# Optimization experiments

Measured on AMD Instinct MI355X. Metric: run time of the kernel, lower is better.

The kernel has to match this reference:

```python
import jax, jax.numpy as jnp
import numpy as np

S, L, T, E, H = 512, 5, 20, 768, 64


def setup_inputs() -> dict:
    key = jax.random.key(0)
    ks = jax.random.split(key, 32)

    def p(k, shape, scale=0.05):
        return jax.random.normal(k, shape, dtype=jnp.float32) * scale

    return {
        "text_input": jax.random.normal(ks[0], (S, L, T, E), dtype=jnp.float32),
        "time_inputs": jax.random.uniform(ks[1], (S, L, T), dtype=jnp.float32),
        # TimeLSTM per-stock params (gate order f, i, o, c_tmp)
        "Wall": p(ks[2], (S, H, 4 * H)), "bWall": p(ks[3], (S, 4 * H)),
        "Uall": p(ks[4], (S, E, 4 * H)), "bUall": p(ks[5], (S, 4 * H)),
        "Wd": p(ks[6], (S, H, H)), "bWd": p(ks[7], (S, H)),
        # shared text/day Attention per stock
        "W1": p(ks[8], (S, H, H)), "b1": p(ks[9], (S, H)),
        "W2": p(ks[10], (S, H, H)), "b2": p(ks[11], (S, H)),
        "V": p(ks[12], (S, H, 1)), "bV": p(ks[13], (S, 1)),
        # day nn.LSTM per stock (gate order i, f, g, o)
        "Wih": p(ks[14], (S, H, 4 * H)), "Whh": p(ks[15], (S, H, 4 * H)),
        "bih": p(ks[16], (S, 4 * H)), "bhh": p(ks[17], (S, 4 * H)),
        # shared output head
        "lin_w": p(ks[18], (H, 1)), "lin_b": p(ks[19], (1,)),
        "no_stocks": S,
    }


def _forward(text_input, time_inputs, Wall, bWall, Uall, bUall, Wd, bWd,
             W1, b1, W2, b2, V, bV, Wih, Whh, bih, bhh, lin_w, lin_b, no_stocks):
    def per_stock(x, ts, Wall, bWall, Uall, bUall, Wd, bWd,
                  W1, b1, W2, b2, V, bV, Wih, Whh, bih, bhh):
        # x: [L, T, E], ts: [L, T] -- lookback days are an inner batch for the TimeLSTM
        u = jnp.einsum('lte,eg->ltg', x, Uall) + bUall  # [L, T, 4H]

        def step(carry, inp):
            h, c = carry                 # [L, H]
            u_t, ts_t = inp              # [L, 4H], [L]
            c_s1 = jnp.tanh(c @ Wd + bWd)
            c_adj = (c - c_s1) + c_s1 * ts_t[:, None]
            gates = h @ Wall + bWall + u_t
            f, i, o, c_tmp = jnp.split(gates, 4, axis=1)
            f = jax.nn.sigmoid(f)
            i = jax.nn.sigmoid(i)
            o = jax.nn.sigmoid(o)
            c_tmp = jax.nn.sigmoid(c_tmp)  # sigmoid (not tanh), faithful to source
            c_new = f * c_adj + i * c_tmp
            h_new = o * jnp.tanh(c_new)
            return (h_new, c_new), o     # module collects the o gate as 'outputs'

        init = (jnp.zeros((L, H), x.dtype), jnp.zeros((L, H), x.dtype))
        (h_fin, _), o_seq = jax.lax.scan(step, init, (u.transpose(1, 0, 2), ts.T))
        full = o_seq.transpose(1, 0, 2)  # [L, T, H]

        # text attention: score = V(tanh(W1(last) + W2(full))), softmax over T
        score = jnp.tanh((h_fin @ W1 + b1)[:, None, :] + full @ W2 + b2) @ V + bV  # [L, T, 1]
        aw = jax.nn.softmax(score, axis=1)
        text_vec = jnp.sum(aw * full, axis=1)  # [L, H]

        # day nn.LSTM: input (1, L, H) seq-first => one cell step with batch=L, zero state
        h0 = jnp.zeros((L, H), x.dtype)
        g = text_vec @ Wih + bih + h0 @ Whh + bhh
        gi, gf, gg, go = jnp.split(g, 4, axis=1)
        c_d = jax.nn.sigmoid(gi) * jnp.tanh(gg)  # f * c0 = 0
        h_d = jax.nn.sigmoid(go) * jnp.tanh(c_d)  # [L, H]; output == h_n here

        # day attention reuses the SAME text_attention weights; full == last == h_d
        s2 = jnp.tanh(h_d @ W1 + b1 + h_d @ W2 + b2) @ V + bV  # [L, 1]
        aw2 = jax.nn.softmax(s2, axis=0)
        return jnp.sum(aw2 * h_d, axis=0)  # [H]

    ft_vec = jax.vmap(per_stock)(text_input, time_inputs, Wall, bWall, Uall, bUall,
                                 Wd, bWd, W1, b1, W2, b2, V, bV,
                                 Wih, Whh, bih, bhh)  # [S, H]
    return jax.nn.leaky_relu(ft_vec @ lin_w + lin_b, negative_slope=0.01)  # [S, 1]


def reference(text_input, time_inputs, Wall, bWall, Uall, bUall, Wd, bWd,
              W1, b1, W2, b2, V, bV, Wih, Whh, bih, bhh, lin_w, lin_b, no_stocks):
    return _forward(text_input, time_inputs, Wall, bWall, Uall, bUall, Wd, bWd,
                    W1, b1, W2, b2, V, bV, Wih, Whh, bih, bhh, lin_w, lin_b, no_stocks)
```

## Files before the change

kernel.cpp:

```cpp
#include <hip/hip_runtime.h>
#include <cstddef>

#define NS 512
#define NL 5
#define NT 20
#define NE 768
#define NH 64
#define NG 256

__device__ __forceinline__ float sigf(float x) { return 1.0f / (1.0f + expf(-x)); }
__device__ __forceinline__ float bcast(float v, int k) {
    return __int_as_float(__builtin_amdgcn_readlane(__float_as_int(v), k));
}

typedef __attribute__((ext_vector_type(8))) short short8v;
typedef __attribute__((ext_vector_type(4))) float f32x4;

__device__ __forceinline__ void split_bf16(float x, unsigned short& hi, unsigned short& lo) {
    unsigned int bx = __float_as_uint(x);
    unsigned int h = (bx + 0x8000u) >> 16;
    hi = (unsigned short)h;
    float r = x - __uint_as_float(h << 16);
    lo = (unsigned short)((__float_as_uint(r) + 0x8000u) >> 16);
}

__global__ __launch_bounds__(512, 2) void k_gemm_u(
    const float* __restrict__ x, const float* __restrict__ U,
    const float* __restrict__ bU, float* __restrict__ u)
{
    __shared__ unsigned short Af[8 * 2 * 64 * 8];
    __shared__ unsigned short Bf[16 * 2 * 64 * 8];
    const int s = blockIdx.x;
    const int tid = threadIdx.x;
    const int wave = tid >> 6, lane = tid & 63;
    const int wm = wave & 1, wn = wave >> 1;
    const float* xg = x + (size_t)s * (NL * NT * NE);
    const float* Ug = U + (size_t)s * (NE * NG);

    f32x4 acc[4][4] = {};

    const int arow = tid >> 2, ab = tid & 3;
    const unsigned int a_off0 = (((unsigned)(arow >> 4) * 2 + 0) * 64 + ((arow & 15) + 16 * ab)) * 8;
    const unsigned int a_off1 = a_off0 + 64 * 8;
    const int bcol = tid & 255, bq1 = tid >> 8;
    const unsigned int b_base = (unsigned)(bcol >> 4) * 2 * 64 * 8;
    const unsigned int b_off1h = b_base + ((bcol & 15) + 16 * bq1) * 8;
    const unsigned int b_off1l = b_off1h + 64 * 8;
    const unsigned int b_off2h = b_base + ((bcol & 15) + 16 * (bq1 + 2)) * 8;
    const unsigned int b_off2l = b_off2h + 64 * 8;

    float av[8], bv1[8], bv2[8];
    {
        const float* pa = xg + (size_t)arow * NE + ab * 8;
        if (arow < 100) {
            float4 q0 = *(const float4*)pa, q1 = *(const float4*)(pa + 4);
            av[0]=q0.x; av[1]=q0.y; av[2]=q0.z; av[3]=q0.w;
            av[4]=q1.x; av[5]=q1.y; av[6]=q1.z; av[7]=q1.w;
        } else {
            #pragma unroll
            for (int j = 0; j < 8; ++j) av[j] = 0.0f;
        }
        const float* pb = Ug + bcol;
        #pragma unroll
        for (int j = 0; j < 8; ++j) {
            bv1[j] = pb[(size_t)(8 * bq1 + j) * NG];
            bv2[j] = pb[(size_t)(8 * bq1 + 16 + j) * NG];
        }
    }

    for (int st = 0; st < 24; ++st) {
        {
            unsigned short h[8], l[8];
            #pragma unroll
            for (int j = 0; j < 8; ++j) split_bf16(av[j], h[j], l[j]);
            uint4 ph, pl;
            ph.x = h[0] | (h[1] << 16); ph.y = h[2] | (h[3] << 16);
            ph.z = h[4] | (h[5] << 16); ph.w = h[6] | (h[7] << 16);
            pl.x = l[0] | (l[1] << 16); pl.y = l[2] | (l[3] << 16);
            pl.z = l[4] | (l[5] << 16); pl.w = l[6] | (l[7] << 16);
            *(uint4*)&Af[a_off0] = ph;
            *(uint4*)&Af[a_off1] = pl;
            #pragma unroll
            for (int j = 0; j < 8; ++j) split_bf16(bv1[j], h[j], l[j]);
            ph.x = h[0] | (h[1] << 16); ph.y = h[2] | (h[3] << 16);
            ph.z = h[4] | (h[5] << 16); ph.w = h[6] | (h[7] << 16);
            pl.x = l[0] | (l[1] << 16); pl.y = l[2] | (l[3] << 16);
            pl.z = l[4] | (l[5] << 16); pl.w = l[6] | (l[7] << 16);
            *(uint4*)&Bf[b_off1h] = ph;
            *(uint4*)&Bf[b_off1l] = pl;
            #pragma unroll
            for (int j = 0; j < 8; ++j) split_bf16(bv2[j], h[j], l[j]);
            ph.x = h[0] | (h[1] << 16); ph.y = h[2] | (h[3] << 16);
            ph.z = h[4] | (h[5] << 16); ph.w = h[6] | (h[7] << 16);
            pl.x = l[0] | (l[1] << 16); pl.y = l[2] | (l[3] << 16);
            pl.z = l[4] | (l[5] << 16); pl.w = l[6] | (l[7] << 16);
            *(uint4*)&Bf[b_off2h] = ph;
            *(uint4*)&Bf[b_off2l] = pl;
        }
        __syncthreads();

        if (st + 1 < 24) {
            const int k0 = (st + 1) * 32;
            const float* pa = xg + (size_t)arow * NE + k0 + ab * 8;
            if (arow < 100) {
                float4 q0 = *(const float4*)pa, q1 = *(const float4*)(pa + 4);
                av[0]=q0.x; av[1]=q0.y; av[2]=q0.z; av[3]=q0.w;
                av[4]=q1.x; av[5]=q1.y; av[6]=q1.z; av[7]=q1.w;
            } else {
                #pragma unroll
                for (int j = 0; j < 8; ++j) av[j] = 0.0f;
            }
            const float* pb = Ug + (size_t)k0 * NG + bcol;
            #pragma unroll
            for (int j = 0; j < 8; ++j) {
                bv1[j] = pb[(size_t)(8 * bq1 + j) * NG];
                bv2[j] = pb[(size_t)(8 * bq1 + 16 + j) * NG];
            }
        }

        short8v ah[4], al[4];
        #pragma unroll
        for (int mi = 0; mi < 4; ++mi) {
            const unsigned int mt = wm * 4 + mi;
            ah[mi] = *(const short8v*)&Af[(mt * 2 + 0) * 512 + lane * 8];
            al[mi] = *(const short8v*)&Af[(mt * 2 + 1) * 512 + lane * 8];
        }
        #pragma unroll
        for (int ni = 0; ni < 4; ++ni) {
            const unsigned int nt = wn * 4 + ni;
            short8v bh = *(const short8v*)&Bf[(nt * 2 + 0) * 512 + lane * 8];
            short8v bl = *(const short8v*)&Bf[(nt * 2 + 1) * 512 + lane * 8];
            #pragma unroll
            for (int mi = 0; mi < 4; ++mi) {
                acc[mi][ni] = __builtin_amdgcn_mfma_f32_16x16x32_bf16(ah[mi], bh, acc[mi][ni], 0, 0, 0);
                acc[mi][ni] = __builtin_amdgcn_mfma_f32_16x16x32_bf16(ah[mi], bl, acc[mi][ni], 0, 0, 0);
                acc[mi][ni] = __builtin_amdgcn_mfma_f32_16x16x32_bf16(al[mi], bh, acc[mi][ni], 0, 0, 0);
            }
        }
        __syncthreads();
    }

    const int c_sub = 4 * (lane >> 4);
    #pragma unroll
    for (int ni = 0; ni < 4; ++ni) {
        const int gcol = wn * 64 + ni * 16 + (lane & 15);
        const float bb = bU[(size_t)s * NG + gcol];
        #pragma unroll
        for (int mi = 0; mi < 4; ++mi) {
            const int grow0 = wm * 64 + mi * 16 + c_sub;
            #pragma unroll
            for (int r = 0; r < 4; ++r) {
                const int grow = grow0 + r;
                if (grow < 100) {
                    const int ld = grow / 20, td = grow % 20;
                    u[(((size_t)s * NT + td) * NL + ld) * NG + gcol] = acc[mi][ni][r] + bb;
                }
            }
        }
    }
}

#define R_WD    0
#define R_GATES 4096
#define R_HS    5376
#define R_TS    5696
#define R_TOT   5796

__global__ __launch_bounds__(320, 4) void k_recur(
    float* __restrict__ u, const float* __restrict__ ti,
    const float* __restrict__ Wall, const float* __restrict__ bWall,
    const float* __restrict__ Wd, const float* __restrict__ bWd)
{
    __shared__ float sm[R_TOT];
    const int s = blockIdx.x;
    const int tid = threadIdx.x;
    const int lq = tid >> 6, hh = tid & 63;
    const int lane = hh;
    float* ug = u + (size_t)s * NT * NL * NG;

    for (int i = tid; i < 1024; i += 320)
        *(float4*)&sm[R_WD + i * 4] = *(const float4*)(Wd + (size_t)s * 4096 + i * 4);
    if (tid < NL * NT) sm[R_TS + tid] = ti[(size_t)s * NL * NT + tid];
    sm[R_HS + tid] = 0.0f;
    const float bwd_r = bWd[(size_t)s * NH + hh];
    float c_reg = 0.0f;
    float wall_r[NH];
    float bwall_r = 0.0f, uc[NL];
    if (tid < NG) {
        bwall_r = bWall[(size_t)s * NG + tid];
        const float* wp = Wall + (size_t)s * (NH * NG) + tid;
        #pragma unroll
        for (int k = 0; k < NH; ++k) wall_r[k] = wp[(size_t)k * NG];
        #pragma unroll
        for (int l = 0; l < NL; ++l) uc[l] = ug[(size_t)l * NG + tid];
    }
    __syncthreads();

    for (int t = 0; t < NT; ++t) {
        float un[NL];
        if (tid < NG) {
            if (t + 1 < NT) {
                #pragma unroll
                for (int l = 0; l < NL; ++l)
                    un[l] = ug[(size_t)((t + 1) * NL + l) * NG + tid];
            } else {
                #pragma unroll
                for (int l = 0; l < NL; ++l) un[l] = 0.0f;
            }
            float hreg[NL];
            #pragma unroll
            for (int l = 0; l < NL; ++l) hreg[l] = sm[R_HS + l * NH + lane];
            float gv[NL];
            #pragma unroll
            for (int l = 0; l < NL; ++l) gv[l] = bwall_r + uc[l];
            #pragma unroll
            for (int k = 0; k < NH; ++k) {
                float w = wall_r[k];
                #pragma unroll
                for (int l = 0; l < NL; ++l)
                    gv[l] += bcast(hreg[l], k) * w;
            }
            #pragma unroll
            for (int l = 0; l < NL; ++l)
                sm[R_GATES + l * NG + tid] = sigf(gv[l]);
        }
        float ssum = bwd_r;
        #pragma unroll
        for (int k = 0; k < NH; ++k)
            ssum += bcast(c_reg, k) * sm[R_WD + k * NH + hh];
        float cs1 = tanhf(ssum);
        float ca = c_reg - cs1 + cs1 * sm[R_TS + lq * NT + t];
        __syncthreads();
        {
            float f  = sm[R_GATES + lq * NG + hh];
            float ii = sm[R_GATES + lq * NG + 64 + hh];
            float oo = sm[R_GATES + lq * NG + 128 + hh];
            float ct = sm[R_GATES + lq * NG + 192 + hh];
            float cn = f * ca + ii * ct;
            c_reg = cn;
            sm[R_HS + tid] = oo * tanhf(cn);
            ug[(size_t)(t * NL + lq) * NG + hh] = oo;
        }
        __syncthreads();
        if (tid < NG) {
            #pragma unroll
            for (int l = 0; l < NL; ++l) uc[l] = un[l];
        }
    }
    ug[(size_t)(0 * NL + lq) * NG + 64 + hh] = sm[R_HS + tid];
}

#define P_W1    0
#define P_W2    4096
#define P_FULLO 8192
#define P_HS    14592
#define P_TQ    14912
#define P_CA    15232
#define P_SC    15552
#define P_B0    15652
#define P_B1    15716
#define P_BVV   15780
#define P_BV1   15844
#define P_TOT   15848

__global__ __launch_bounds__(320, 2) void k_post(
    const float* __restrict__ u,
    const float* __restrict__ W1, const float* __restrict__ b1,
    const float* __restrict__ W2, const float* __restrict__ b2,
    const float* __restrict__ V, const float* __restrict__ bV,
    const float* __restrict__ Wih, const float* __restrict__ bih,
    const float* __restrict__ bhh, const float* __restrict__ lin_w,
    const float* __restrict__ lin_b, float* __restrict__ out)
{
    __shared__ float sm[P_TOT];
    const int s = blockIdx.x;
    const int tid = threadIdx.x;
    const int lq = tid >> 6, hh = tid & 63;
    const int lane = hh;
    const float* ug = u + (size_t)s * NT * NL * NG;

    for (int i = tid; i < 1024; i += 320)
        *(float4*)&sm[P_W1 + i * 4] = *(const float4*)(W1 + (size_t)s * 4096 + i * 4);
    for (int i = tid; i < 1024; i += 320)
        *(float4*)&sm[P_W2 + i * 4] = *(const float4*)(W2 + (size_t)s * 4096 + i * 4);
    for (int i = tid; i < 1600; i += 320) {
        const int idx = i >> 4;
        const int l = idx / NT, t = idx % NT;
        const int k4 = (i & 15) * 4;
        *(float4*)&sm[P_FULLO + idx * NH + k4] =
            *(const float4*)(ug + (size_t)(t * NL + l) * NG + k4);
    }
    sm[P_HS + tid] = ug[(size_t)(0 * NL + lq) * NG + 64 + hh];
    if (tid < NH) {
        sm[P_B0 + tid]  = b1[(size_t)s * NH + tid];
        sm[P_B1 + tid]  = b2[(size_t)s * NH + tid];
        sm[P_BVV + tid] = V[(size_t)s * NH + tid];
    }
    if (tid == 0) sm[P_BV1] = bV[s];
    __syncthreads();

    {
        float qv = sm[P_B0 + hh];
        for (int k4 = 0; k4 < NH; k4 += 4) {
            float4 hv = *(const float4*)&sm[P_HS + lq * NH + k4];
            qv += hv.x * sm[P_W1 + (k4 + 0) * NH + hh]
                + hv.y * sm[P_W1 + (k4 + 1) * NH + hh]
                + hv.z * sm[P_W1 + (k4 + 2) * NH + hh]
                + hv.w * sm[P_W1 + (k4 + 3) * NH + hh];
        }
        sm[P_TQ + tid] = qv;
    }
    __syncthreads();

    for (int lt = lq; lt < NL * NT; lt += 5) {
        int l = lt / NT;
        float v = sm[P_TQ + l * NH + lane] + sm[P_B1 + lane];
        for (int k4 = 0; k4 < NH; k4 += 4) {
            float4 fv = *(const float4*)&sm[P_FULLO + lt * NH + k4];
            v += fv.x * sm[P_W2 + (k4 + 0) * NH + lane]
               + fv.y * sm[P_W2 + (k4 + 1) * NH + lane]
               + fv.z * sm[P_W2 + (k4 + 2) * NH + lane]
               + fv.w * sm[P_W2 + (k4 + 3) * NH + lane];
        }
        v = tanhf(v) * sm[P_BVV + lane];
        #pragma unroll
        for (int m = 32; m > 0; m >>= 1) v += __shfl_xor(v, m, 64);
        if (lane == 0) sm[P_SC + lt] = v + sm[P_BV1];
    }
    __syncthreads();

    if (tid < NL) {
        float mx = -1e30f;
        for (int t = 0; t < NT; ++t) mx = fmaxf(mx, sm[P_SC + tid * NT + t]);
        float sum = 0.0f;
        for (int t = 0; t < NT; ++t) {
            float e = expf(sm[P_SC + tid * NT + t] - mx);
            sm[P_SC + tid * NT + t] = e;
            sum += e;
        }
        float inv = 1.0f / sum;
        for (int t = 0; t < NT; ++t) sm[P_SC + tid * NT + t] *= inv;
    }
    __syncthreads();

    {
        float sv = 0.0f;
        #pragma unroll
        for (int t = 0; t < NT; ++t)
            sv += sm[P_SC + lq * NT + t] * sm[P_FULLO + (lq * NT + t) * NH + hh];
        sm[P_CA + tid] = sv;
    }
    __syncthreads();

    if (tid < NG) {
        float bsum = bih[(size_t)s * NG + tid] + bhh[(size_t)s * NG + tid];
        float d[NL];
        #pragma unroll
        for (int l = 0; l < NL; ++l) d[l] = bsum;
        for (int k = 0; k < NH; ++k) {
            float wk = Wih[((size_t)s * NH + k) * NG + tid];
            #pragma unroll
            for (int l = 0; l < NL; ++l)
                d[l] += sm[P_CA + l * NH + k] * wk;
        }
        #pragma unroll
        for (int l = 0; l < NL; ++l)
            sm[P_FULLO + l * NG + tid] = d[l];
    }
    __syncthreads();
    {
        float gi = sm[P_FULLO + lq * NG + hh];
        float gg = sm[P_FULLO + lq * NG + 128 + hh];
        float go = sm[P_FULLO + lq * NG + 192 + hh];
        float cd = sigf(gi) * tanhf(gg);
        sm[P_TQ + tid] = sigf(go) * tanhf(cd);
    }
    __syncthreads();

    {
        float v = sm[P_B0 + lane] + sm[P_B1 + lane];
        for (int k4 = 0; k4 < NH; k4 += 4) {
            float4 hv = *(const float4*)&sm[P_TQ + lq * NH + k4];
            v += hv.x * (sm[P_W1 + (k4 + 0) * NH + lane] + sm[P_W2 + (k4 + 0) * NH + lane])
               + hv.y * (sm[P_W1 + (k4 + 1) * NH + lane] + sm[P_W2 + (k4 + 1) * NH + lane])
               + hv.z * (sm[P_W1 + (k4 + 2) * NH + lane] + sm[P_W2 + (k4 + 2) * NH + lane])
               + hv.w * (sm[P_W1 + (k4 + 3) * NH + lane] + sm[P_W2 + (k4 + 3) * NH + lane]);
        }
        v = tanhf(v) * sm[P_BVV + lane];
        #pragma unroll
        for (int m = 32; m > 0; m >>= 1) v += __shfl_xor(v, m, 64);
        if (lane == 0) sm[P_SC + lq] = v + sm[P_BV1];
    }
    __syncthreads();
    if (tid == 0) {
        float mx = -1e30f;
        for (int l = 0; l < NL; ++l) mx = fmaxf(mx, sm[P_SC + l]);
        float sum = 0.0f;
        for (int l = 0; l < NL; ++l) {
            float e = expf(sm[P_SC + l] - mx);
            sm[P_SC + l] = e;
            sum += e;
        }
        float inv = 1.0f / sum;
        for (int l = 0; l < NL; ++l) sm[P_SC + l] *= inv;
    }
    __syncthreads();

    if (tid < NH) {
        float fv = 0.0f;
        #pragma unroll
        for (int l = 0; l < NL; ++l)
            fv += sm[P_SC + l] * sm[P_TQ + l * NH + tid];
        fv *= lin_w[tid];
        #pragma unroll
        for (int m = 32; m > 0; m >>= 1) fv += __shfl_xor(fv, m, 64);
        if (tid == 0) {
            float val = fv + lin_b[0];
            out[s] = val > 0.0f ? val : 0.01f * val;
        }
    }
}

extern "C" void kernel_launch(void* const* d_in, const int* in_sizes, int n_in,
                              void* d_out, int out_size, void* d_ws, size_t ws_size,
                              hipStream_t stream) {
    (void)in_sizes; (void)n_in; (void)out_size; (void)ws_size;
    const float* x     = (const float*)d_in[0];
    const float* ti    = (const float*)d_in[1];
    const float* Wall  = (const float*)d_in[2];
    const float* bWall = (const float*)d_in[3];
    const float* Uall  = (const float*)d_in[4];
    const float* bUall = (const float*)d_in[5];
    const float* Wd    = (const float*)d_in[6];
    const float* bWd   = (const float*)d_in[7];
    const float* W1    = (const float*)d_in[8];
    const float* b1    = (const float*)d_in[9];
    const float* W2    = (const float*)d_in[10];
    const float* b2    = (const float*)d_in[11];
    const float* V     = (const float*)d_in[12];
    const float* bV    = (const float*)d_in[13];
    const float* Wih   = (const float*)d_in[14];
    const float* bih   = (const float*)d_in[16];
    const float* bhh   = (const float*)d_in[17];
    const float* lin_w = (const float*)d_in[18];
    const float* lin_b = (const float*)d_in[19];
    float* out = (float*)d_out;
    float* u = (float*)d_ws;

    k_gemm_u<<<NS, 512, 0, stream>>>(x, Uall, bUall, u);
    k_recur<<<NS, 320, 0, stream>>>(u, ti, Wall, bWall, Wd, bWd);
    k_post<<<NS, 320, 0, stream>>>(u, W1, b1, W2, b2, V, bV,
                                   Wih, bih, bhh, lin_w, lin_b, out);
}
```

Measured before the change: 879.5 us.

## Split U-GEMM across two blocks, use fp16 split MFMA, LDS broadcasts in recurrence

The input-projection GEMM now runs two blocks per stock, each computing half of the 256 gate columns. This doubles the grid and raises launch_bounds occupancy to 4 blocks per CU. The hi/lo operand split moves from manual bf16 rounding to packed fp16 conversion (cvt_pkrtz) with fp16 MFMA, which cuts conversion ALU work and gives more mantissa bits, at some risk of fp16 range overflow. In the recurrence, readlane broadcasts of h and c are replaced by float4 LDS reads, with c kept in shared memory. This adds LDS traffic but removes the serial readlane chains.

New measurement: 873.1 us. Within noise of the previous version (-0.7%).

```diff
diff --git a/kernel.cpp b/kernel.cpp
--- a/kernel.cpp
+++ b/kernel.cpp
@@ -9,47 +9,54 @@
 #define NG 256
 
 __device__ __forceinline__ float sigf(float x) { return 1.0f / (1.0f + expf(-x)); }
-__device__ __forceinline__ float bcast(float v, int k) {
-    return __int_as_float(__builtin_amdgcn_readlane(__float_as_int(v), k));
-}
-
-typedef __attribute__((ext_vector_type(8))) short short8v;
+
+typedef __fp16 h16x2 __attribute__((ext_vector_type(2)));
+typedef _Float16 f16x8 __attribute__((ext_vector_type(8)));
 typedef __attribute__((ext_vector_type(4))) float f32x4;
 
-__device__ __forceinline__ void split_bf16(float x, unsigned short& hi, unsigned short& lo) {
-    unsigned int bx = __float_as_uint(x);
-    unsigned int h = (bx + 0x8000u) >> 16;
-    hi = (unsigned short)h;
-    float r = x - __uint_as_float(h << 16);
-    lo = (unsigned short)((__float_as_uint(r) + 0x8000u) >> 16);
-}
-
-__global__ __launch_bounds__(512, 2) void k_gemm_u(
+union PkU { h16x2 h; unsigned u; };
+
+__device__ __forceinline__ void split_pk(float a, float b, unsigned& hi, unsigned& lo) {
+    PkU H, L;
+    H.h = __builtin_amdgcn_cvt_pkrtz(a, b);
+    float ra = a - (float)H.h[0];
+    float rb = b - (float)H.h[1];
+    L.h = __builtin_amdgcn_cvt_pkrtz(ra, rb);
+    hi = H.u; lo = L.u;
+}
+
+__device__ __forceinline__ void stage8(const float v[8], unsigned short* base, unsigned off) {
+    uint4 ph, pl;
+    split_pk(v[0], v[1], ph.x, pl.x);
+    split_pk(v[2], v[3], ph.y, pl.y);
+    split_pk(v[4], v[5], ph.z, pl.z);
+    split_pk(v[6], v[7], ph.w, pl.w);
+    *(uint4*)&base[off]       = ph;
+    *(uint4*)&base[off + 512] = pl;
+}
+
+__global__ __launch_bounds__(512, 4) void k_gemm_u(
     const float* __restrict__ x, const float* __restrict__ U,
     const float* __restrict__ bU, float* __restrict__ u)
 {
-    __shared__ unsigned short Af[8 * 2 * 64 * 8];
-    __shared__ unsigned short Bf[16 * 2 * 64 * 8];
-    const int s = blockIdx.x;
+    __shared__ unsigned short Af[8 * 2 * 512];
+    __shared__ unsigned short Bf[8 * 2 * 512];
+    const int bid = blockIdx.x;
+    const int s = bid >> 1, half = bid & 1;
     const int tid = threadIdx.x;
     const int wave = tid >> 6, lane = tid & 63;
     const int wm = wave & 1, wn = wave >> 1;
     const float* xg = x + (size_t)s * (NL * NT * NE);
-    const float* Ug = U + (size_t)s * (NE * NG);
-
-    f32x4 acc[4][4] = {};
+    const float* Ug = U + (size_t)s * (NE * NG) + half * 128;
+
+    f32x4 acc[4][2] = {};
 
     const int arow = tid >> 2, ab = tid & 3;
-    const unsigned int a_off0 = (((unsigned)(arow >> 4) * 2 + 0) * 64 + ((arow & 15) + 16 * ab)) * 8;
-    const unsigned int a_off1 = a_off0 + 64 * 8;
-    const int bcol = tid & 255, bq1 = tid >> 8;
-    const unsigned int b_base = (unsigned)(bcol >> 4) * 2 * 64 * 8;
-    const unsigned int b_off1h = b_base + ((bcol & 15) + 16 * bq1) * 8;
-    const unsigned int b_off1l = b_off1h + 64 * 8;
-    const unsigned int b_off2h = b_base + ((bcol & 15) + 16 * (bq1 + 2)) * 8;
-    const unsigned int b_off2l = b_off2h + 64 * 8;
-
-    float av[8], bv1[8], bv2[8];
+    const unsigned a_off = ((unsigned)(arow >> 4) * 2) * 512 + ((arow & 15) + 16 * ab) * 8;
+    const int bcol = tid & 127, bkq = tid >> 7;
+    const unsigned b_off = ((unsigned)(bcol >> 4) * 2) * 512 + ((bcol & 15) + 16 * bkq) * 8;
+
+    float av[8], bv[8];
     {
         const float* pa = xg + (size_t)arow * NE + ab * 8;
         if (arow < 100) {
@@ -60,43 +67,14 @@
             #pragma unroll
             for (int j = 0; j < 8; ++j) av[j] = 0.0f;
         }
-        const float* pb = Ug + bcol;
-        #pragma unroll
-        for (int j = 0; j < 8; ++j) {
-            bv1[j] = pb[(size_t)(8 * bq1 + j) * NG];
-            bv2[j] = pb[(size_t)(8 * bq1 + 16 + j) * NG];
-        }
+        #pragma unroll
+        for (int j = 0; j < 8; ++j)
+            bv[j] = Ug[(size_t)(8 * bkq + j) * NG + bcol];
     }
 
     for (int st = 0; st < 24; ++st) {
-        {
-            unsigned short h[8], l[8];
-            #pragma unroll
-            for (int j = 0; j < 8; ++j) split_bf16(av[j], h[j], l[j]);
-            uint4 ph, pl;
-            ph.x = h[0] | (h[1] << 16); ph.y = h[2] | (h[3] << 16);
-            ph.z = h[4] | (h[5] << 16); ph.w = h[6] | (h[7] << 16);
-            pl.x = l[0] | (l[1] << 16); pl.y = l[2] | (l[3] << 16);
-            pl.z = l[4] | (l[5] << 16); pl.w = l[6] | (l[7] << 16);
-            *(uint4*)&Af[a_off0] = ph;
-            *(uint4*)&Af[a_off1] = pl;
-            #pragma unroll
-            for (int j = 0; j < 8; ++j) split_bf16(bv1[j], h[j], l[j]);
-            ph.x = h[0] | (h[1] << 16); ph.y = h[2] | (h[3] << 16);
-            ph.z = h[4] | (h[5] << 16); ph.w = h[6] | (h[7] << 16);
-            pl.x = l[0] | (l[1] << 16); pl.y = l[2] | (l[3] << 16);
-            pl.z = l[4] | (l[5] << 16); pl.w = l[6] | (l[7] << 16);
-            *(uint4*)&Bf[b_off1h] = ph;
-            *(uint4*)&Bf[b_off1l] = pl;
-            #pragma unroll
-            for (int j = 0; j < 8; ++j) split_bf16(bv2[j], h[j], l[j]);
-            ph.x = h[0] | (h[1] << 16); ph.y = h[2] | (h[3] << 16);
-            ph.z = h[4] | (h[5] << 16); ph.w = h[6] | (h[7] << 16);
-            pl.x = l[0] | (l[1] << 16); pl.y = l[2] | (l[3] << 16);
-            pl.z = l[4] | (l[5] << 16); pl.w = l[6] | (l[7] << 16);
-            *(uint4*)&Bf[b_off2h] = ph;
-            *(uint4*)&Bf[b_off2l] = pl;
-        }
+        stage8(av, Af, a_off);
+        stage8(bv, Bf, b_off);
         __syncthreads();
 
         if (st + 1 < 24) {
@@ -110,31 +88,28 @@
                 #pragma unroll
                 for (int j = 0; j < 8; ++j) av[j] = 0.0f;
             }
-            const float* pb = Ug + (size_t)k0 * NG + bcol;
-            #pragma unroll
-            for (int j = 0; j < 8; ++j) {
-                bv1[j] = pb[(size_t)(8 * bq1 + j) * NG];
-                bv2[j] = pb[(size_t)(8 * bq1 + 16 + j) * NG];
-            }
-        }
-
-        short8v ah[4], al[4];
+            #pragma unroll
+            for (int j = 0; j < 8; ++j)
+                bv[j] = Ug[(size_t)(k0 + 8 * bkq + j) * NG + bcol];
+        }
+
+        f16x8 bh[2], bl[2];
+        #pragma unroll
+        for (int ni = 0; ni < 2; ++ni) {
+            const unsigned nt = wn * 2 + ni;
+            bh[ni] = *(const f16x8*)&Bf[(nt * 2 + 0) * 512 + lane * 8];
+            bl[ni] = *(const f16x8*)&Bf[(nt * 2 + 1) * 512 + lane * 8];
+        }
         #pragma unroll
         for (int mi = 0; mi < 4; ++mi) {
-            const unsigned int mt = wm * 4 + mi;
-            ah[mi] = *(const short8v*)&Af[(mt * 2 + 0) * 512 + lane * 8];
-            al[mi] = *(const short8v*)&Af[(mt * 2 + 1) * 512 + lane * 8];
-        }
-        #pragma unroll
-        for (int ni = 0; ni < 4; ++ni) {
-            const unsigned int nt = wn * 4 + ni;
-            short8v bh = *(const short8v*)&Bf[(nt * 2 + 0) * 512 + lane * 8];
-            short8v bl = *(const short8v*)&Bf[(nt * 2 + 1) * 512 + lane * 8];
-            #pragma unroll
-            for (int mi = 0; mi < 4; ++mi) {
-                acc[mi][ni] = __builtin_amdgcn_mfma_f32_16x16x32_bf16(ah[mi], bh, acc[mi][ni], 0, 0, 0);
-                acc[mi][ni] = __builtin_amdgcn_mfma_f32_16x16x32_bf16(ah[mi], bl, acc[mi][ni], 0, 0, 0);
-                acc[mi][ni] = __builtin_amdgcn_mfma_f32_16x16x32_bf16(al[mi], bh, acc[mi][ni], 0, 0, 0);
+            const unsigned mt = wm * 4 + mi;
+            f16x8 ah = *(const f16x8*)&Af[(mt * 2 + 0) * 512 + lane * 8];
+            f16x8 al = *(const f16x8*)&Af[(mt * 2 + 1) * 512 + lane * 8];
+            #pragma unroll
+            for (int ni = 0; ni < 2; ++ni) {
+                acc[mi][ni] = __builtin_amdgcn_mfma_f32_16x16x32_f16(ah, bh[ni], acc[mi][ni], 0, 0, 0);
+                acc[mi][ni] = __builtin_amdgcn_mfma_f32_16x16x32_f16(ah, bl[ni], acc[mi][ni], 0, 0, 0);
+                acc[mi][ni] = __builtin_amdgcn_mfma_f32_16x16x32_f16(al, bh[ni], acc[mi][ni], 0, 0, 0);
             }
         }
         __syncthreads();
@@ -142,8 +117,8 @@
 
     const int c_sub = 4 * (lane >> 4);
     #pragma unroll
-    for (int ni = 0; ni < 4; ++ni) {
-        const int gcol = wn * 64 + ni * 16 + (lane & 15);
+    for (int ni = 0; ni < 2; ++ni) {
+        const int gcol = half * 128 + (wn * 2 + ni) * 16 + (lane & 15);
         const float bb = bU[(size_t)s * NG + gcol];
         #pragma unroll
         for (int mi = 0; mi < 4; ++mi) {
@@ -163,8 +138,9 @@
 #define R_WD    0
 #define R_GATES 4096
 #define R_HS    5376
-#define R_TS    5696
-#define R_TOT   5796
+#define R_CS    5696
+#define R_TS    6016
+#define R_TOT   6116
 
 __global__ __launch_bounds__(320, 4) void k_recur(
     float* __restrict__ u, const float* __restrict__ ti,
@@ -175,15 +151,14 @@
     const int s = blockIdx.x;
     const int tid = threadIdx.x;
     const int lq = tid >> 6, hh = tid & 63;
-    const int lane = hh;
     float* ug = u + (size_t)s * NT * NL * NG;
 
     for (int i = tid; i < 1024; i += 320)
         *(float4*)&sm[R_WD + i * 4] = *(const float4*)(Wd + (size_t)s * 4096 + i * 4);
     if (tid < NL * NT) sm[R_TS + tid] = ti[(size_t)s * NL * NT + tid];
     sm[R_HS + tid] = 0.0f;
+    sm[R_CS + tid] = 0.0f;
     const float bwd_r = bWd[(size_t)s * NH + hh];
-    float c_reg = 0.0f;
     float wall_r[NH];
     float bwall_r = 0.0f, uc[NL];
     if (tid < NG) {
@@ -207,29 +182,35 @@
                 #pragma unroll
                 for (int l = 0; l < NL; ++l) un[l] = 0.0f;
             }
-            float hreg[NL];
-            #pragma unroll
-            for (int l = 0; l < NL; ++l) hreg[l] = sm[R_HS + l * NH + lane];
             float gv[NL];
             #pragma unroll
             for (int l = 0; l < NL; ++l) gv[l] = bwall_r + uc[l];
-            #pragma unroll
-            for (int k = 0; k < NH; ++k) {
-                float w = wall_r[k];
+            for (int k4 = 0; k4 < NH; k4 += 4) {
+                const float w0 = wall_r[k4 + 0];
+                const float w1 = wall_r[k4 + 1];
+                const float w2 = wall_r[k4 + 2];
+                const float w3 = wall_r[k4 + 3];
                 #pragma unroll
-                for (int l = 0; l < NL; ++l)
-                    gv[l] += bcast(hreg[l], k) * w;
+                for (int l = 0; l < NL; ++l) {
+                    float4 hv = *(const float4*)&sm[R_HS + l * NH + k4];
+                    gv[l] += hv.x * w0 + hv.y * w1 + hv.z * w2 + hv.w * w3;
+                }
             }
             #pragma unroll
             for (int l = 0; l < NL; ++l)
                 sm[R_GATES + l * NG + tid] = sigf(gv[l]);
         }
+        const float cold = sm[R_CS + tid];
         float ssum = bwd_r;
-        #pragma unroll
-        for (int k = 0; k < NH; ++k)
-            ssum += bcast(c_reg, k) * sm[R_WD + k * NH + hh];
-        float cs1 = tanhf(ssum);
-        float ca = c_reg - cs1 + cs1 * sm[R_TS + lq * NT + t];
+        for (int k4 = 0; k4 < NH; k4 += 4) {
+            float4 cv = *(const float4*)&sm[R_CS + lq * NH + k4];
+            ssum += cv.x * sm[R_WD + (k4 + 0) * NH + hh]
+                  + cv.y * sm[R_WD + (k4 + 1) * NH + hh]
+                  + cv.z * sm[R_WD + (k4 + 2) * NH + hh]
+                  + cv.w * sm[R_WD + (k4 + 3) * NH + hh];
+        }
+        const float cs1 = tanhf(ssum);
+        const float ca = cold - cs1 + cs1 * sm[R_TS + lq * NT + t];
         __syncthreads();
         {
             float f  = sm[R_GATES + lq * NG + hh];
@@ -237,7 +218,7 @@
             float oo = sm[R_GATES + lq * NG + 128 + hh];
             float ct = sm[R_GATES + lq * NG + 192 + hh];
             float cn = f * ca + ii * ct;
-            c_reg = cn;
+            sm[R_CS + tid] = cn;
             sm[R_HS + tid] = oo * tanhf(cn);
             ug[(size_t)(t * NL + lq) * NG + hh] = oo;
         }
@@ -447,7 +428,7 @@
     float* out = (float*)d_out;
     float* u = (float*)d_ws;
 
-    k_gemm_u<<<NS, 512, 0, stream>>>(x, Uall, bUall, u);
+    k_gemm_u<<<NS * 2, 512, 0, stream>>>(x, Uall, bUall, u);
     k_recur<<<NS, 320, 0, stream>>>(u, ti, Wall, bWall, Wd, bWd);
     k_post<<<NS, 320, 0, stream>>>(u, W1, b1, W2, b2, V, bV,
                                    Wih, bih, bhh, lin_w, lin_b, out);
```
